# Kernel tuning notes

Hardware: AMD Instinct MI355X
Metric: run time of the kernel (lower is better)

Reference implementation:

```python
import jax, jax.numpy as jnp
import numpy as np

FEATURE_DIM = 68
ONE_HOT_MAX = 29  # one-hot coordinate features only for coords < 29


def _compute_encodings(height, width):
    # height, width are static Python ints
    xs = jnp.arange(width, dtype=jnp.float32)
    ys = jnp.arange(height, dtype=jnp.float32)

    def axis_feats(coords, size):
        if size > 1:
            norm = 2.0 * (coords / (size - 1)) - 1.0
            angle = jnp.pi * (coords / (size - 1))
        else:
            norm = jnp.zeros_like(coords)
            angle = jnp.zeros_like(coords)
        sign = jnp.sign(coords - size / 2.0)  # -1 / 0 / +1 around midpoint
        rtan = jnp.round(jnp.tan(angle))
        return jnp.stack([norm, sign, jnp.sin(angle), jnp.cos(angle), rtan], axis=-1)  # [size, 5]

    xf = axis_feats(xs, width)    # [W, 5] -> feature slots 0,2,4,6,8
    yf = axis_feats(ys, height)   # [H, 5] -> feature slots 1,3,5,7,9

    xb = jnp.broadcast_to(xf[None, :, :], (height, width, 5))
    yb = jnp.broadcast_to(yf[:, None, :], (height, width, 5))
    # interleave x/y features -> order x0,y0,x1,y1,... matches slots 0..9
    first10 = jnp.stack([xb, yb], axis=-1).reshape(height, width, 10)

    idx = jnp.arange(ONE_HOT_MAX)
    ohx = (xs[:, None] == idx[None, :]).astype(jnp.float32)  # [W, 29], zero rows for x >= 29
    ohy = (ys[:, None] == idx[None, :]).astype(jnp.float32)  # [H, 29]
    ohx_b = jnp.broadcast_to(ohx[None, :, :], (height, width, ONE_HOT_MAX))
    ohy_b = jnp.broadcast_to(ohy[:, None, :], (height, width, ONE_HOT_MAX))

    return jnp.concatenate([first10, ohx_b, ohy_b], axis=-1)  # [H, W, 68]


def setup_inputs() -> dict:
    key = jax.random.key(0)
    H, W, B = 512, 512, 8
    x = jax.random.normal(key, (B, H * W), dtype=jnp.float32)
    return {"x": x, "height": H, "width": W}


def reference(x, height, width):
    batch_size, seq_len = x.shape
    enc = _compute_encodings(height, width).reshape(-1, FEATURE_DIM)  # [H*W, 68]
    enc_b = jnp.broadcast_to(enc[None, :, :], (batch_size, seq_len, FEATURE_DIM))
    return jnp.concatenate([x[..., None], enc_b], axis=-1)  # [B, H*W, 69]
```

## Files before the change

### kernel.cpp

```cpp
#include <hip/hip_runtime.h>
#include <math.h>

typedef float f32x4 __attribute__((ext_vector_type(4)));

#define NF 69u
#define WROWS 32u
#define WTILE_FLOATS (WROWS * NF)
#define WTILE_F4 (WTILE_FLOATS / 4u)
#define NCHUNK 9u
#define BLOCK 256u
#define WAVES 4u

__global__ void pe_table_kernel(const int* __restrict__ hptr,
                                const int* __restrict__ wptr,
                                float* __restrict__ tab8) {
    const int H = *hptr;
    const int W = *wptr;
    const int total = W + H;
    for (int i = (int)(blockIdx.x * blockDim.x + threadIdx.x); i < total;
         i += (int)(gridDim.x * blockDim.x)) {
        const bool is_y = (i >= W);
        const int c = is_y ? (i - W) : i;
        const int size = is_y ? H : W;
        double norm = 0.0, angle = 0.0;
        if (size > 1) {
            const double r = (double)c / (double)(size - 1);
            norm = 2.0 * r - 1.0;
            angle = M_PI * r;
        }
        const double d = (double)c - 0.5 * (double)size;
        const float sgn = (d > 0.0) ? 1.0f : ((d < 0.0) ? -1.0f : 0.0f);
        const int base = (is_y ? 8 * W : 0) + 8 * c;
        tab8[base + 0] = (float)norm;
        tab8[base + 1] = sgn;
        tab8[base + 2] = (float)sin(angle);
        tab8[base + 3] = (float)cos(angle);
        tab8[base + 4] = (float)rint(tan(angle));
    }
}

__global__ __launch_bounds__(BLOCK) void pe_main_kernel(
    const float* __restrict__ x,
    const int* __restrict__ hptr, const int* __restrict__ wptr,
    const float* __restrict__ tab8,
    float* __restrict__ out, unsigned int Q ) {
    __shared__ __align__(16) float lds[WAVES][WTILE_FLOATS];

    const unsigned int W = (unsigned int)*wptr;
    const unsigned int H = (unsigned int)*hptr;
    const unsigned int yoff8 = 8u * W;
    const unsigned int lane = threadIdx.x & 63u;
    const unsigned int wid = threadIdx.x >> 6;
    const unsigned int r = lane & 31u;
    const bool hi = lane >= 32u;
    float* buf = lds[wid];
    float* row = buf + r * NF;

    {
        f32x4 z = {0.f, 0.f, 0.f, 0.f};
        f32x4* bp = (f32x4*)buf;
        for (unsigned int j = lane; j < WTILE_F4; j += 64u) bp[j] = z;
    }

    const unsigned int ntiles = (Q + WROWS - 1u) / WROWS;
    const unsigned int gw = blockIdx.x * WAVES + wid;
    const unsigned int nw = gridDim.x * WAVES;

    for (unsigned int T = gw; T < ntiles; T += nw) {
        const unsigned int q = T * WROWS + r;
        unsigned int w = 0u, h = 0u;
        const bool valid = q < Q;
        if (valid) {
            const unsigned int t = q / W;
            w = q - t * W;
            h = t - (t / H) * H;
            if (!hi) {
                const f32x4 xa = *(const f32x4*)(tab8 + 8u * w);
                const float xa4 = tab8[8u * w + 4u];
                row[0] = x[q];
                row[1] = xa[0]; row[3] = xa[1];
                row[5] = xa[2]; row[7] = xa[3];
                row[9] = xa4;
            } else {
                const f32x4 ya = *(const f32x4*)(tab8 + yoff8 + 8u * h);
                const float ya4 = tab8[yoff8 + 8u * h + 4u];
                row[2] = ya[0]; row[4]  = ya[1];
                row[6] = ya[2]; row[8]  = ya[3];
                row[10] = ya4;
                if (w < 29u) row[11u + w] = 1.0f;
                if (h < 29u) row[40u + h] = 1.0f;
            }
        }

        const unsigned int rem = Q - T * WROWS;
        const size_t obase = (size_t)T * (size_t)WTILE_FLOATS;
        const f32x4* lp = (const f32x4*)buf;
        f32x4* op = (f32x4*)(out + obase);

        if (rem >= WROWS) {
            f32x4 v[NCHUNK];
#pragma unroll
            for (unsigned int j = 0u; j < NCHUNK; ++j) {
                const unsigned int idx = lane + 64u * j;
                if (j < NCHUNK - 1u || idx < WTILE_F4) v[j] = lp[idx];
            }
#pragma unroll
            for (unsigned int j = 0u; j < NCHUNK; ++j) {
                const unsigned int idx = lane + 64u * j;
                if (j < NCHUNK - 1u || idx < WTILE_F4) op[idx] = v[j];
            }
        } else {
            const unsigned int nfl = rem * NF;
            const unsigned int n4 = nfl >> 2;
            for (unsigned int j = lane; j < n4; j += 64u) op[j] = lp[j];
            for (unsigned int j = (n4 << 2) + lane; j < nfl; j += 64u)
                out[obase + j] = buf[j];
        }

        if (valid && hi) {
            if (w < 29u) row[11u + w] = 0.0f;
            if (h < 29u) row[40u + h] = 0.0f;
        }
    }
}

extern "C" void kernel_launch(void* const* d_in, const int* in_sizes, int n_in,
                              void* d_out, int out_size, void* d_ws, size_t ws_size,
                              hipStream_t stream) {
    const float* x = (const float*)d_in[0];
    const int* hptr = (const int*)d_in[1];
    const int* wptr = (const int*)d_in[2];
    float* out = (float*)d_out;
    float* tab8 = (float*)d_ws;

    pe_table_kernel<<<8, 256, 0, stream>>>(hptr, wptr, tab8);

    const unsigned int Q = (unsigned int)in_sizes[0];
    const unsigned int ntiles = (Q + WROWS - 1u) / WROWS;
    unsigned int blocks = (ntiles + WAVES - 1u) / WAVES;
    if (blocks > 2048u) blocks = 2048u;
    if (blocks == 0u) blocks = 1u;
    pe_main_kernel<<<blocks, BLOCK, 0, stream>>>(x, hptr, wptr, tab8, out, Q);
}
```

Before: 120.7 us.

## Compute output elements directly in registers instead of staging rows in LDS

Replaces the per-wave LDS staging of 32-row tiles with direct computation: each thread owns a float4 of a 64-row block tile, decodes row and feature from a precomputed pattern, and computes each element from x, the small table, or the one-hot compare. It also adds a power-of-two fast path for the coordinate division. This removes LDS writes and reads and the zero/reset bookkeeping, but adds per-element branching and scattered small table loads.

```diff
diff --git a/kernel.cpp b/kernel.cpp
--- a/kernel.cpp
+++ b/kernel.cpp
@@ -4,12 +4,11 @@
 typedef float f32x4 __attribute__((ext_vector_type(4)));
 
 #define NF 69u
-#define WROWS 32u
-#define WTILE_FLOATS (WROWS * NF)
-#define WTILE_F4 (WTILE_FLOATS / 4u)
-#define NCHUNK 9u
+#define TROWS 64u
+#define TILE_FLOATS (TROWS * NF)
+#define TILE_F4 (TILE_FLOATS / 4u)
 #define BLOCK 256u
-#define WAVES 4u
+#define NCH 5u
 
 __global__ void pe_table_kernel(const int* __restrict__ hptr,
                                 const int* __restrict__ wptr,
@@ -39,87 +38,97 @@
     }
 }
 
+__device__ __forceinline__ void pe_coords(unsigned int q, unsigned int W,
+                                          unsigned int H, bool pot,
+                                          unsigned int lw,
+                                          unsigned int& w, unsigned int& h) {
+    if (pot) {
+        w = q & (W - 1u);
+        h = (q >> lw) & (H - 1u);
+    } else {
+        const unsigned int t = q / W;
+        w = q - t * W;
+        h = t % H;
+    }
+}
+
+__device__ __forceinline__ float pe_elem(unsigned int fm, unsigned int qq,
+                                         unsigned int wq, unsigned int hq,
+                                         const float* __restrict__ x,
+                                         const float* __restrict__ tab8,
+                                         unsigned int yoff8) {
+    float val = ((fm >= 11u && fm < 40u && wq == fm - 11u) ||
+                 (fm >= 40u && hq == fm - 40u)) ? 1.0f : 0.0f;
+    if (fm <= 10u) {
+        if (fm == 0u) {
+            val = x[qq];
+        } else {
+            const unsigned int g = fm - 1u;
+            val = (g & 1u) ? tab8[yoff8 + 8u * hq + (g >> 1)]
+                           : tab8[8u * wq + (g >> 1)];
+        }
+    }
+    return val;
+}
+
 __global__ __launch_bounds__(BLOCK) void pe_main_kernel(
     const float* __restrict__ x,
     const int* __restrict__ hptr, const int* __restrict__ wptr,
     const float* __restrict__ tab8,
     float* __restrict__ out, unsigned int Q ) {
-    __shared__ __align__(16) float lds[WAVES][WTILE_FLOATS];
-
     const unsigned int W = (unsigned int)*wptr;
     const unsigned int H = (unsigned int)*hptr;
     const unsigned int yoff8 = 8u * W;
-    const unsigned int lane = threadIdx.x & 63u;
-    const unsigned int wid = threadIdx.x >> 6;
-    const unsigned int r = lane & 31u;
-    const bool hi = lane >= 32u;
-    float* buf = lds[wid];
-    float* row = buf + r * NF;
+    const bool pot = ((W & (W - 1u)) == 0u) && ((H & (H - 1u)) == 0u);
+    const unsigned int lw = pot ? (unsigned int)(31 - __clz((int)W)) : 0u;
+    const unsigned int tid = threadIdx.x;
+    const unsigned int ntiles = (Q + TROWS - 1u) / TROWS;
+    const size_t total = (size_t)Q * NF;
 
-    {
-        f32x4 z = {0.f, 0.f, 0.f, 0.f};
-        f32x4* bp = (f32x4*)buf;
-        for (unsigned int j = lane; j < WTILE_F4; j += 64u) bp[j] = z;
+    unsigned int pat[NCH];
+#pragma unroll
+    for (unsigned int j = 0u; j < NCH; ++j) {
+        const unsigned int local = tid + BLOCK * j;
+        const unsigned int ff = 4u * local;
+        pat[j] = ((ff / 69u) << 8) | (ff % 69u);
     }
 
-    const unsigned int ntiles = (Q + WROWS - 1u) / WROWS;
-    const unsigned int gw = blockIdx.x * WAVES + wid;
-    const unsigned int nw = gridDim.x * WAVES;
-
-    for (unsigned int T = gw; T < ntiles; T += nw) {
-        const unsigned int q = T * WROWS + r;
-        unsigned int w = 0u, h = 0u;
-        const bool valid = q < Q;
-        if (valid) {
-            const unsigned int t = q / W;
-            w = q - t * W;
-            h = t - (t / H) * H;
-            if (!hi) {
-                const f32x4 xa = *(const f32x4*)(tab8 + 8u * w);
-                const float xa4 = tab8[8u * w + 4u];
-                row[0] = x[q];
-                row[1] = xa[0]; row[3] = xa[1];
-                row[5] = xa[2]; row[7] = xa[3];
-                row[9] = xa4;
+    for (unsigned int T = blockIdx.x; T < ntiles; T += gridDim.x) {
+        const size_t basef = (size_t)T * TILE_FLOATS;
+        const unsigned int Trow = T * TROWS;
+        const bool full = basef + TILE_FLOATS <= total;
+#pragma unroll
+        for (unsigned int j = 0u; j < NCH; ++j) {
+            const unsigned int local = tid + BLOCK * j;
+            if (j == NCH - 1u && local >= TILE_F4) continue;
+            const unsigned int row = pat[j] >> 8;
+            const unsigned int f0 = pat[j] & 0xFFu;
+            const unsigned int q = Trow + row;
+            unsigned int w0, h0, w1, h1;
+            pe_coords(q, W, H, pot, lw, w0, h0);
+            pe_coords(q + 1u, W, H, pot, lw, w1, h1);
+            f32x4 v;
+#pragma unroll
+            for (unsigned int e = 0u; e < 4u; ++e) {
+                const unsigned int ff = f0 + e;
+                const bool wr = ff >= NF;
+                const unsigned int fm = wr ? ff - NF : ff;
+                const unsigned int qq = wr ? q + 1u : q;
+                const unsigned int wq = wr ? w1 : w0;
+                const unsigned int hq = wr ? h1 : h0;
+                v[e] = (full || basef + 4u * local + e < total)
+                           ? pe_elem(fm, qq, wq, hq, x, tab8, yoff8)
+                           : 0.0f;
+            }
+            if (full) {
+                *(f32x4*)(out + basef + 4u * local) = v;
             } else {
-                const f32x4 ya = *(const f32x4*)(tab8 + yoff8 + 8u * h);
-                const float ya4 = tab8[yoff8 + 8u * h + 4u];
-                row[2] = ya[0]; row[4]  = ya[1];
-                row[6] = ya[2]; row[8]  = ya[3];
-                row[10] = ya4;
-                if (w < 29u) row[11u + w] = 1.0f;
-                if (h < 29u) row[40u + h] = 1.0f;
+#pragma unroll
+                for (unsigned int e = 0u; e < 4u; ++e) {
+                    const size_t idx = basef + 4u * local + e;
+                    if (idx < total) out[idx] = v[e];
+                }
             }
-        }
-
-        const unsigned int rem = Q - T * WROWS;
-        const size_t obase = (size_t)T * (size_t)WTILE_FLOATS;
-        const f32x4* lp = (const f32x4*)buf;
-        f32x4* op = (f32x4*)(out + obase);
-
-        if (rem >= WROWS) {
-            f32x4 v[NCHUNK];
-#pragma unroll
-            for (unsigned int j = 0u; j < NCHUNK; ++j) {
-                const unsigned int idx = lane + 64u * j;
-                if (j < NCHUNK - 1u || idx < WTILE_F4) v[j] = lp[idx];
-            }
-#pragma unroll
-            for (unsigned int j = 0u; j < NCHUNK; ++j) {
-                const unsigned int idx = lane + 64u * j;
-                if (j < NCHUNK - 1u || idx < WTILE_F4) op[idx] = v[j];
-            }
-        } else {
-            const unsigned int nfl = rem * NF;
-            const unsigned int n4 = nfl >> 2;
-            for (unsigned int j = lane; j < n4; j += 64u) op[j] = lp[j];
-            for (unsigned int j = (n4 << 2) + lane; j < nfl; j += 64u)
-                out[obase + j] = buf[j];
-        }
-
-        if (valid && hi) {
-            if (w < 29u) row[11u + w] = 0.0f;
-            if (h < 29u) row[40u + h] = 0.0f;
         }
     }
 }
@@ -136,9 +145,8 @@
     pe_table_kernel<<<8, 256, 0, stream>>>(hptr, wptr, tab8);
 
     const unsigned int Q = (unsigned int)in_sizes[0];
-    const unsigned int ntiles = (Q + WROWS - 1u) / WROWS;
-    unsigned int blocks = (ntiles + WAVES - 1u) / WAVES;
-    if (blocks > 2048u) blocks = 2048u;
+    const unsigned int ntiles = (Q + TROWS - 1u) / TROWS;
+    unsigned int blocks = ntiles < 2048u ? ntiles : 2048u;
     if (blocks == 0u) blocks = 1u;
     pe_main_kernel<<<blocks, BLOCK, 0, stream>>>(x, hptr, wptr, tab8, out, Q);
 }
```

Result: slower. 253.2 us (+109.7%).
